# Optimization experiments

Hardware: AMD Instinct MI355X
Metric: run time of the kernel (lower is better)

Reference implementation:

```python
import jax, jax.numpy as jnp
import numpy as np

H = 512          # hidden_dim
AA = 21          # aa_num
NF = 6165        # num_features
B, N = 4, 2048   # graphs per batch, nodes per graph
LAMB = 1.0
OUT = 2


def gcn(x, adj, W, b):
    # Kipf GCN with self-loops on a (weighted) dense adjacency [B,n,n].
    n = adj.shape[-1]
    A = adj + jnp.eye(n, dtype=adj.dtype)
    d = jnp.sum(A, axis=-1)
    dinv = jax.lax.rsqrt(jnp.maximum(d, 1e-12))
    xw = x @ W                              # [B,n,Hout]
    msg = dinv[..., :, None] * (A @ (dinv[..., :, None] * xw))
    return msg + b


def hgpsl_pool(x, adj, att):
    # Node information score ||(I - D^-1 A) X||_1 (HGP-SL), top-k ratio 0.5,
    # then structure learning: row-softmax of pairwise attention + lamb*A.
    B_, n, h = x.shape
    d = jnp.sum(adj, axis=-1)
    dinv = 1.0 / jnp.maximum(d, 1.0)
    prop = (dinv[..., :, None] * adj) @ x
    score = jnp.sum(jnp.abs(x - prop), axis=-1)          # [B,n]
    k = n // 2
    _, idx = jax.lax.top_k(score, k)                     # [B,k]
    xk = jnp.take_along_axis(x, idx[:, :, None], axis=1)             # [B,k,h]
    a1 = jnp.take_along_axis(adj, idx[:, :, None], axis=1)           # [B,k,n]
    adjk = jnp.take_along_axis(a1, idx[:, None, :], axis=2)          # [B,k,k]
    # structure learning: e_ij = a^T [x_i || x_j] + lamb * A_ij
    li = xk @ att[:h]                                    # [B,k]
    lj = xk @ att[h:]                                    # [B,k]
    logits = li[:, :, None] + lj[:, None, :] + LAMB * adjk
    new_adj = jax.nn.softmax(logits, axis=-1)            # [B,k,k]
    return xk, new_adj


def readout(x):
    return jnp.concatenate([jnp.max(x, axis=1), jnp.mean(x, axis=1)], axis=-1)


def setup_inputs() -> dict:
    key = jax.random.key(0)
    ks = jax.random.split(key, 16)
    x = jax.random.normal(ks[0], (B, N, NF), dtype=jnp.float32)
    u = jax.random.uniform(ks[1], (B, N, N), dtype=jnp.float32)
    adj = (u < 0.008).astype(jnp.float32)
    adj = jnp.maximum(adj, jnp.swapaxes(adj, 1, 2))
    adj = adj * (1.0 - jnp.eye(N, dtype=jnp.float32))
    def w(k, shape):
        fan = shape[0]
        return jax.random.normal(k, shape, dtype=jnp.float32) / np.sqrt(fan)
    return {
        "x": x, "adj": adj,
        "lin1_W": w(ks[2], (NF - AA, H)), "lin1_b": jnp.zeros((H,), jnp.float32),
        "lin2_W": w(ks[3], (AA, AA)),     "lin2_b": jnp.zeros((AA,), jnp.float32),
        "conv1_W": w(ks[4], (H + AA, H)), "conv1_b": jnp.zeros((H,), jnp.float32),
        "conv2_W": w(ks[5], (H, H)),      "conv2_b": jnp.zeros((H,), jnp.float32),
        "conv3_W": w(ks[6], (H, H)),      "conv3_b": jnp.zeros((H,), jnp.float32),
        "att1": w(ks[7], (2 * H,)), "att2": w(ks[8], (2 * H,)),
        "fc1_W": w(ks[9], (2 * H, H)),    "fc1_b": jnp.zeros((H,), jnp.float32),
        "fc2_W": w(ks[10], (H, H // 2)),  "fc2_b": jnp.zeros((H // 2,), jnp.float32),
        "fc3_W": w(ks[11], (H // 2, OUT)),"fc3_b": jnp.zeros((OUT,), jnp.float32),
    }


def reference(x, adj, lin1_W, lin1_b, lin2_W, lin2_b, conv1_W, conv1_b,
              conv2_W, conv2_b, conv3_W, conv3_b, att1, att2,
              fc1_W, fc1_b, fc2_W, fc2_b, fc3_W, fc3_b):
    relu = jax.nn.relu
    x1 = relu(x[..., AA:] @ lin1_W + lin1_b)   # [B,N,H]
    x2 = relu(x[..., :AA] @ lin2_W + lin2_b)   # [B,N,AA]
    h = jnp.concatenate([x2, x1], axis=-1)     # [B,N,H+AA]
    h = relu(gcn(h, adj, conv1_W, conv1_b))
    h, adj1 = hgpsl_pool(h, adj, att1)         # N -> N/2
    r1 = readout(h)
    h = relu(gcn(h, adj1, conv2_W, conv2_b))
    h, adj2 = hgpsl_pool(h, adj1, att2)        # N/2 -> N/4
    r2 = readout(h)
    h = relu(gcn(h, adj2, conv3_W, conv3_b))
    r3 = readout(h)
    z = relu(r1) + relu(r2) + relu(r3)         # [B,2H]
    z = relu(z @ fc1_W + fc1_b)                # dropout is eval-mode identity
    z = relu(z @ fc2_W + fc2_b)
    return jax.nn.log_softmax(z @ fc3_W + fc3_b, axis=-1)
```

## Files before the change

kernel.cpp:

```cpp
#include <hip/hip_runtime.h>
#include <cstdint>
#include <cstddef>

typedef __bf16 bf16x8 __attribute__((ext_vector_type(8)));
typedef float f32x4 __attribute__((ext_vector_type(4)));

#define BUFSZ 24576

template <int MF>
__global__ __launch_bounds__(256) void gemm_mfma(
    const float* __restrict__ A, long lda, long sAb,
    const __bf16* __restrict__ Bp, long sBpb,
    float* __restrict__ C, long ldc, long sCb,
    int M, int N, int K,
    const float* __restrict__ bias,
    const float* __restrict__ rowscale,
    const float* __restrict__ addm, long sAddb, long ldadd,
    int do_relu)
{
  constexpr int BM = 32 * MF;
  __shared__ __align__(16) char smem[2 * BUFSZ];

  const int bz = blockIdx.z;
  const float* Ab = A + (size_t)bz * sAb;
  const __bf16* Bb = Bp + (size_t)bz * sBpb;
  float* Cb = C + (size_t)bz * sCb;

  int flat = blockIdx.y * gridDim.x + blockIdx.x;
  const int nwg = gridDim.x * gridDim.y;
  if ((nwg & 7) == 0) { const int q = nwg >> 3; flat = (flat & 7) * q + (flat >> 3); }
  const int col0 = (flat % gridDim.x) * 128;
  const int row0 = (flat / gridDim.x) * BM;

  const int t = threadIdx.x;
  const int w = t >> 6, l = t & 63;
  const int l16 = l & 15, lq = l >> 4;
  const int wr = w >> 1, wc = w & 1;
  const int T = K >> 5;

  const int s_row = t >> 2, s_oct = t & 3;
  const int a_off = (s_row >> 4) * 1024 + (s_oct * 16 + (s_row & 15)) * 16;
  const float* aptr = Ab + (size_t)(row0 + s_row) * lda + s_oct * 8;

  const __bf16* bsrc[4];
#pragma unroll
  for (int j = 0; j < 4; ++j) {
    const int c = t + 256 * j;
    const int g = c >> 7;
    bsrc[j] = Bb + ((size_t)((col0 >> 4) + g) * T) * 1024 + (size_t)(c & 127) * 8;
  }

  f32x4 acc[MF][4];
#pragma unroll
  for (int i = 0; i < MF; ++i)
#pragma unroll
    for (int j = 0; j < 4; ++j) acc[i][j] = (f32x4){0.f, 0.f, 0.f, 0.f};

  float a0r[8], a1r[8];
  bf16x8 bs0[4], bs1[4];

#define GA(dst, K0)                                                         \
  { const float* ap = aptr + (K0);                                          \
    _Pragma("unroll") for (int i = 0; i < 8; ++i) dst[i] = ap[i]; }

#define GB(dst, KT)                                                         \
  { _Pragma("unroll") for (int j = 0; j < 4; ++j)                           \
      dst[j] = *(const bf16x8*)(bsrc[j] + (size_t)(KT) * 1024); }

#define WA(buf, src)                                                        \
  { char* wb = smem + (buf) * BUFSZ; bf16x8 vh, vl;                         \
    _Pragma("unroll") for (int i = 0; i < 8; ++i) {                         \
      const __bf16 hh = (__bf16)src[i];                                     \
      vh[i] = hh; vl[i] = (__bf16)(src[i] - (float)hh); }                   \
    *(bf16x8*)(wb + a_off) = vh;                                            \
    *(bf16x8*)(wb + 4096 + a_off) = vl; }

#define WB(buf, src)                                                        \
  { char* wb = smem + (buf) * BUFSZ + 8192;                                 \
    _Pragma("unroll") for (int j = 0; j < 4; ++j)                           \
      *(bf16x8*)(wb + (t + 256 * j) * 16) = src[j]; }

#define COMPUTE(buf)                                                        \
  { const char* rb = smem + (buf) * BUFSZ;                                  \
    bf16x8 fbh[4], fbl[4];                                                  \
    _Pragma("unroll") for (int nf = 0; nf < 4; ++nf) {                      \
      const int g = wc * 4 + nf;                                            \
      fbh[nf] = *(const bf16x8*)(rb + 8192 + g * 2048 + l * 16);            \
      fbl[nf] = *(const bf16x8*)(rb + 8192 + g * 2048 + 1024 + l * 16); }   \
    _Pragma("unroll") for (int mf = 0; mf < MF; ++mf) {                     \
      const int fg = wr * MF + mf;                                          \
      bf16x8 fh = *(const bf16x8*)(rb + fg * 1024 + l * 16);                \
      bf16x8 fl = *(const bf16x8*)(rb + 4096 + fg * 1024 + l * 16);         \
      _Pragma("unroll") for (int nf = 0; nf < 4; ++nf) {                    \
        acc[mf][nf] = __builtin_amdgcn_mfma_f32_16x16x32_bf16(fl, fbh[nf], acc[mf][nf], 0, 0, 0); \
        acc[mf][nf] = __builtin_amdgcn_mfma_f32_16x16x32_bf16(fh, fbl[nf], acc[mf][nf], 0, 0, 0); \
        acc[mf][nf] = __builtin_amdgcn_mfma_f32_16x16x32_bf16(fh, fbh[nf], acc[mf][nf], 0, 0, 0); } } }

  GA(a0r, 0); GB(bs0, 0);
  WA(0, a0r); WB(0, bs0);
  if (T > 1) GA(a1r, 32);
  __syncthreads();

  int kt = 0;
  for (; kt + 2 <= T; kt += 2) {
    if (kt + 2 < T) GA(a0r, (kt + 2) * 32);
    GB(bs1, kt + 1);
    COMPUTE(0);
    WA(1, a1r); WB(1, bs1);
    __syncthreads();
    if (kt + 3 < T) GA(a1r, (kt + 3) * 32);
    if (kt + 2 < T) GB(bs0, kt + 2);
    COMPUTE(1);
    if (kt + 2 < T) { WA(0, a0r); WB(0, bs0); }
    __syncthreads();
  }
  if (kt < T) {
    COMPUTE(0);
  }
#undef GA
#undef GB
#undef WA
#undef WB
#undef COMPUTE

#pragma unroll
  for (int mf = 0; mf < MF; ++mf) {
#pragma unroll
    for (int r = 0; r < 4; ++r) {
      const int row = row0 + wr * (MF * 16) + mf * 16 + lq * 4 + r;
      const float rs = rowscale ? rowscale[(size_t)bz * M + row] : 1.f;
#pragma unroll
      for (int nf = 0; nf < 4; ++nf) {
        const int col = col0 + wc * 64 + nf * 16 + l16;
        float v = acc[mf][nf][r];
        if (addm) v += addm[(size_t)bz * sAddb + (size_t)row * ldadd + col];
        v *= rs;
        if (bias) v += bias[col];
        if (do_relu) v = fmaxf(v, 0.f);
        Cb[(size_t)row * ldc + col] = v;
      }
    }
  }
}

__global__ __launch_bounds__(64) void pack_b_kernel(
    const float* __restrict__ in, long sInb, int Kin, int Nin,
    __bf16* __restrict__ outP, long sPb, int T)
{
  const int kt = blockIdx.x, nf = blockIdx.y, b = blockIdx.z;
  const int l = threadIdx.x;
  const float* src = in + (size_t)b * sInb;
  const int col = nf * 16 + (l & 15);
  const int k0 = kt * 32 + (l >> 4) * 8;
  bf16x8 vh, vl;
#pragma unroll
  for (int j = 0; j < 8; ++j) {
    const int k = k0 + j;
    const float v = (k < Kin) ? src[(size_t)k * Nin + col] : 0.f;
    const __bf16 h = (__bf16)v;
    vh[j] = h; vl[j] = (__bf16)(v - (float)h);
  }
  __bf16* dst = outP + (size_t)b * sPb + ((size_t)nf * T + kt) * 1024 + l * 8;
  *(bf16x8*)dst = vh;
  *(bf16x8*)(dst + 512) = vl;
}

__global__ void lin2_kernel(const float* __restrict__ x, const float* __restrict__ W,
                            const float* __restrict__ b, float* __restrict__ h)
{
  int id = blockIdx.x * blockDim.x + threadIdx.x;
  if (id >= 4 * 2048 * 21) return;
  int row = id / 21, j = id % 21;
  const float* xr = x + (size_t)row * 6165;
  float acc = b[j];
  for (int i = 0; i < 21; ++i) acc = fmaf(xr[i], W[i * 21 + j], acc);
  h[(size_t)row * 544 + j] = fmaxf(acc, 0.f);
}

__global__ void pad_h_kernel(float* __restrict__ h)
{
  int id = blockIdx.x * blockDim.x + threadIdx.x;
  if (id >= 4 * 2048 * 11) return;
  int row = id / 11, c = 533 + id % 11;
  h[(size_t)row * 544 + c] = 0.f;
}

__global__ __launch_bounds__(256) void degrees_kernel(const float* __restrict__ adj,
                                                      float* __restrict__ dg,
                                                      float* __restrict__ dp)
{
  __shared__ float red[256];
  const int row = blockIdx.x;
  const int t = threadIdx.x;
  const float* ar = adj + (size_t)row * 2048;
  float s = 0.f;
  for (int j = t; j < 2048; j += 256) s += ar[j];
  red[t] = s; __syncthreads();
  for (int off = 128; off > 0; off >>= 1) {
    if (t < off) red[t] += red[t + off];
    __syncthreads();
  }
  if (t == 0) {
    float S = red[0];
    dg[row] = rsqrtf(fmaxf(S + 1.f, 1e-12f));
    dp[row] = 1.f / fmaxf(S, 1.f);
  }
}

__global__ __launch_bounds__(256) void conv1_msg_kernel(
    const float* __restrict__ adj, const float* __restrict__ xw,
    const float* __restrict__ dinv, const float* __restrict__ bias,
    float* __restrict__ out)
{
  __shared__ int nbr[2048];
  __shared__ float nval[2048];
  __shared__ int cnts[256];
  const int b = blockIdx.y, i = blockIdx.x, t = threadIdx.x;
  const float* ar = adj + ((size_t)(b * 2048 + i)) * 2048;
  int myj[8]; float myv[8]; int mc = 0;
  const int j0 = t * 8;
#pragma unroll
  for (int q = 0; q < 8; ++q) {
    float v = ar[j0 + q];
    if (v != 0.f) { myj[mc] = j0 + q; myv[mc] = v; ++mc; }
  }
  cnts[t] = mc; __syncthreads();
  for (int off = 1; off < 256; off <<= 1) {
    int v = cnts[t]; int add = (t >= off) ? cnts[t - off] : 0;
    __syncthreads();
    cnts[t] = v + add; __syncthreads();
  }
  const int base = cnts[t] - mc;
  const int total = cnts[255];
  for (int q = 0; q < mc; ++q) { nbr[base + q] = myj[q]; nval[base + q] = myv[q]; }
  __syncthreads();

  const float* xwb = xw + (size_t)b * 2048 * 512;
  const float* dv = dinv + b * 2048;
  float acc0 = 0.f, acc1 = 0.f;
  for (int n = 0; n < total; ++n) {
    const int j = nbr[n];
    const float w = nval[n] * dv[j];
    const float* xr = xwb + (size_t)j * 512;
    acc0 = fmaf(w, xr[t], acc0);
    acc1 = fmaf(w, xr[t + 256], acc1);
  }
  const float di = dv[i];
  const float* xi = xwb + (size_t)i * 512;
  acc0 = fmaf(di, xi[t], acc0);
  acc1 = fmaf(di, xi[t + 256], acc1);
  float* orow = out + ((size_t)(b * 2048 + i)) * 512;
  orow[t]       = fmaxf(di * acc0 + bias[t], 0.f);
  orow[t + 256] = fmaxf(di * acc1 + bias[t + 256], 0.f);
}

__global__ __launch_bounds__(256) void pool1_score_kernel(
    const float* __restrict__ adj, const float* __restrict__ h1,
    const float* __restrict__ dpool, float* __restrict__ score)
{
  __shared__ int nbr[2048];
  __shared__ float nval[2048];
  __shared__ int cnts[256];
  __shared__ float red[256];
  const int b = blockIdx.y, i = blockIdx.x, t = threadIdx.x;
  const float* ar = adj + ((size_t)(b * 2048 + i)) * 2048;
  int myj[8]; float myv[8]; int mc = 0;
  const int j0 = t * 8;
#pragma unroll
  for (int q = 0; q < 8; ++q) {
    float v = ar[j0 + q];
    if (v != 0.f) { myj[mc] = j0 + q; myv[mc] = v; ++mc; }
  }
  cnts[t] = mc; __syncthreads();
  for (int off = 1; off < 256; off <<= 1) {
    int v = cnts[t]; int add = (t >= off) ? cnts[t - off] : 0;
    __syncthreads();
    cnts[t] = v + add; __syncthreads();
  }
  const int base = cnts[t] - mc;
  const int total = cnts[255];
  for (int q = 0; q < mc; ++q) { nbr[base + q] = myj[q]; nval[base + q] = myv[q]; }
  __syncthreads();

  const float* hb = h1 + (size_t)b * 2048 * 512;
  float acc0 = 0.f, acc1 = 0.f;
  for (int n = 0; n < total; ++n) {
    const int j = nbr[n];
    const float w = nval[n];
    const float* xr = hb + (size_t)j * 512;
    acc0 = fmaf(w, xr[t], acc0);
    acc1 = fmaf(w, xr[t + 256], acc1);
  }
  const float dpi = dpool[b * 2048 + i];
  const float* hi = hb + (size_t)i * 512;
  float part = fabsf(hi[t] - dpi * acc0) + fabsf(hi[t + 256] - dpi * acc1);
  red[t] = part; __syncthreads();
  for (int off = 128; off > 0; off >>= 1) {
    if (t < off) red[t] += red[t + off];
    __syncthreads();
  }
  if (t == 0) score[b * 2048 + i] = red[0];
}

__global__ __launch_bounds__(1024) void topk_kernel(
    const float* __restrict__ score, int* __restrict__ idx_out, int n, int k)
{
  __shared__ unsigned long long key[2048];
  const unsigned b = blockIdx.x, t = threadIdx.x;
  const unsigned bd = blockDim.x;
  for (unsigned i = t; i < (unsigned)n; i += bd) {
    unsigned u = __float_as_uint(score[(size_t)b * n + i]);
    key[i] = ((unsigned long long)u << 32) | (unsigned)(~i);
  }
  __syncthreads();
  for (unsigned size = 2; size <= (unsigned)n; size <<= 1) {
    for (unsigned stride = size >> 1; stride > 0; stride >>= 1) {
      const unsigned i = (t / stride) * (stride * 2) + (t % stride);
      const unsigned ixj = i + stride;
      const bool up = ((i & size) == 0);
      unsigned long long a = key[i], c = key[ixj];
      if (up ? (a < c) : (a > c)) { key[i] = c; key[ixj] = a; }
      __syncthreads();
    }
  }
  const unsigned my = ~(unsigned)(key[t] & 0xFFFFFFFFull);
  __syncthreads();
  unsigned* arr = (unsigned*)key;
  arr[t] = my;
  __syncthreads();
  for (unsigned size = 2; size <= (unsigned)k; size <<= 1) {
    for (unsigned stride = size >> 1; stride > 0; stride >>= 1) {
      if (t < (unsigned)k / 2) {
        const unsigned i = (t / stride) * (stride * 2) + (t % stride);
        const unsigned ixj = i + stride;
        const bool up = ((i & size) == 0);
        unsigned a = arr[i], c = arr[ixj];
        if (up ? (a > c) : (a < c)) { arr[i] = c; arr[ixj] = a; }
      }
      __syncthreads();
    }
  }
  idx_out[(size_t)b * k + t] = (int)arr[t];
}

__global__ __launch_bounds__(256) void gather_li_kernel(
    const float* __restrict__ X, int src_n,
    const int* __restrict__ idx, int k,
    const float* __restrict__ att,
    float* __restrict__ xk, float* __restrict__ li, float* __restrict__ lj)
{
  __shared__ float redA[256], redB[256];
  const int b = blockIdx.y, r = blockIdx.x, t = threadIdx.x;
  const int g = idx[(size_t)b * k + r];
  const float* src = X + ((size_t)(b * src_n + g)) * 512;
  float* dst = xk + ((size_t)(b * k + r)) * 512;
  const float v0 = src[t], v1 = src[t + 256];
  dst[t] = v0; dst[t + 256] = v1;
  redA[t] = v0 * att[t] + v1 * att[t + 256];
  redB[t] = v0 * att[512 + t] + v1 * att[512 + t + 256];
  __syncthreads();
  for (int off = 128; off > 0; off >>= 1) {
    if (t < off) { redA[t] += redA[t + off]; redB[t] += redB[t + off]; }
    __syncthreads();
  }
  if (t == 0) { li[(size_t)b * k + r] = redA[0]; lj[(size_t)b * k + r] = redB[0]; }
}

__global__ __launch_bounds__(256) void slearn_kernel(
    const float* __restrict__ Asrc, int src_n,
    const int* __restrict__ idx, int k,
    const float* __restrict__ li, const float* __restrict__ lj,
    float* __restrict__ adj_out, float* __restrict__ dg, float* __restrict__ dp)
{
  __shared__ int gidx[1024];
  __shared__ float ljv[1024];
  __shared__ float lg[1024];
  __shared__ float red[256];
  const int b = blockIdx.y, r = blockIdx.x, t = threadIdx.x;
  for (int j = t; j < k; j += 256) { gidx[j] = idx[(size_t)b * k + j]; ljv[j] = lj[(size_t)b * k + j]; }
  __syncthreads();
  const int gi = gidx[r];
  const float lir = li[(size_t)b * k + r];
  const float* ar = Asrc + ((size_t)(b * src_n + gi)) * src_n;
  float mx = -3.4e38f;
  for (int j = t; j < k; j += 256) {
    float v = lir + ljv[j] + ar[gidx[j]];
    lg[j] = v; mx = fmaxf(mx, v);
  }
  red[t] = mx; __syncthreads();
  for (int off = 128; off > 0; off >>= 1) {
    if (t < off) red[t] = fmaxf(red[t], red[t + off]);
    __syncthreads();
  }
  const float m = red[0]; __syncthreads();
  float sm = 0.f;
  for (int j = t; j < k; j += 256) { float e = expf(lg[j] - m); lg[j] = e; sm += e; }
  red[t] = sm; __syncthreads();
  for (int off = 128; off > 0; off >>= 1) {
    if (t < off) red[t] += red[t + off];
    __syncthreads();
  }
  const float s = red[0]; __syncthreads();
  const float inv = 1.f / s;
  float ps = 0.f;
  float* orow = adj_out + ((size_t)(b * k + r)) * k;
  for (int j = t; j < k; j += 256) { float p = lg[j] * inv; orow[j] = p; ps += p; }
  red[t] = ps; __syncthreads();
  for (int off = 128; off > 0; off >>= 1) {
    if (t < off) red[t] += red[t + off];
    __syncthreads();
  }
  if (t == 0) {
    float S = red[0];
    dg[(size_t)b * k + r] = rsqrtf(fmaxf(S + 1.f, 1e-12f));
    dp[(size_t)b * k + r] = 1.f / fmaxf(S, 1.f);
  }
}

__global__ __launch_bounds__(512) void absdiff_kernel(
    const float* __restrict__ X, const float* __restrict__ P, float* __restrict__ score)
{
  __shared__ float red[512];
  const int row = blockIdx.x, t = threadIdx.x;
  float d = fabsf(X[(size_t)row * 512 + t] - P[(size_t)row * 512 + t]);
  red[t] = d; __syncthreads();
  for (int off = 256; off > 0; off >>= 1) {
    if (t < off) red[t] += red[t + off];
    __syncthreads();
  }
  if (t == 0) score[row] = red[0];
}

__global__ __launch_bounds__(512) void readout_part_kernel(
    const float* __restrict__ X, int nrows, int chunk_rows,
    float* __restrict__ partM, float* __restrict__ partS)
{
  const int b = blockIdx.x, chunk = blockIdx.y, c = threadIdx.x;
  const float* xb = X + ((size_t)b * nrows + (size_t)chunk * chunk_rows) * 512;
  float mx = -3.4e38f, sm = 0.f;
  for (int r = 0; r < chunk_rows; ++r) {
    float v = xb[(size_t)r * 512 + c];
    mx = fmaxf(mx, v); sm += v;
  }
  const size_t o = ((size_t)(b * gridDim.y + chunk)) * 512 + c;
  partM[o] = mx; partS[o] = sm;
}

__global__ __launch_bounds__(512) void readout_comb_kernel(
    const float* __restrict__ partM, const float* __restrict__ partS,
    int nchunks, int nrows, float* __restrict__ out)
{
  const int b = blockIdx.x, c = threadIdx.x;
  float mx = -3.4e38f, sm = 0.f;
  for (int q = 0; q < nchunks; ++q) {
    const size_t o = ((size_t)(b * nchunks + q)) * 512 + c;
    mx = fmaxf(mx, partM[o]); sm += partS[o];
  }
  out[(size_t)b * 1024 + c] = mx;
  out[(size_t)b * 1024 + 512 + c] = sm / (float)nrows;
}

__global__ __launch_bounds__(512) void final_mlp_kernel(
    const float* __restrict__ r1, const float* __restrict__ r2, const float* __restrict__ r3,
    const float* __restrict__ fc1W, const float* __restrict__ fc1b,
    const float* __restrict__ fc2W, const float* __restrict__ fc2b,
    const float* __restrict__ fc3W, const float* __restrict__ fc3b,
    float* __restrict__ out)
{
  __shared__ float z[1024];
  __shared__ float z1[512];
  __shared__ float z2[256];
  __shared__ float l[2];
  const int b = blockIdx.x, t = threadIdx.x;
  for (int c = t; c < 1024; c += 512)
    z[c] = fmaxf(r1[(size_t)b * 1024 + c], 0.f) + fmaxf(r2[(size_t)b * 1024 + c], 0.f)
         + fmaxf(r3[(size_t)b * 1024 + c], 0.f);
  __syncthreads();
  {
    float acc = fc1b[t];
    for (int i = 0; i < 1024; ++i) acc = fmaf(z[i], fc1W[(size_t)i * 512 + t], acc);
    z1[t] = fmaxf(acc, 0.f);
  }
  __syncthreads();
  if (t < 256) {
    float acc = fc2b[t];
    for (int i = 0; i < 512; ++i) acc = fmaf(z1[i], fc2W[(size_t)i * 256 + t], acc);
    z2[t] = fmaxf(acc, 0.f);
  }
  __syncthreads();
  if (t < 2) {
    float acc = fc3b[t];
    for (int i = 0; i < 256; ++i) acc = fmaf(z2[i], fc3W[(size_t)i * 2 + t], acc);
    l[t] = acc;
  }
  __syncthreads();
  if (t == 0) {
    float m = fmaxf(l[0], l[1]);
    float ls = m + logf(expf(l[0] - m) + expf(l[1] - m));
    out[b * 2 + 0] = l[0] - ls;
    out[b * 2 + 1] = l[1] - ls;
  }
}

extern "C" void kernel_launch(void* const* d_in, const int* in_sizes, int n_in,
                              void* d_out, int out_size, void* d_ws, size_t ws_size,
                              hipStream_t stream)
{
  (void)in_sizes; (void)n_in; (void)out_size; (void)ws_size;
  const float* x       = (const float*)d_in[0];
  const float* adj     = (const float*)d_in[1];
  const float* lin1_W  = (const float*)d_in[2];
  const float* lin1_b  = (const float*)d_in[3];
  const float* lin2_W  = (const float*)d_in[4];
  const float* lin2_b  = (const float*)d_in[5];
  const float* conv1_W = (const float*)d_in[6];
  const float* conv1_b = (const float*)d_in[7];
  const float* conv2_W = (const float*)d_in[8];
  const float* conv2_b = (const float*)d_in[9];
  const float* conv3_W = (const float*)d_in[10];
  const float* conv3_b = (const float*)d_in[11];
  const float* att1    = (const float*)d_in[12];
  const float* att2    = (const float*)d_in[13];
  const float* fc1_W   = (const float*)d_in[14];
  const float* fc1_b   = (const float*)d_in[15];
  const float* fc2_W   = (const float*)d_in[16];
  const float* fc2_b   = (const float*)d_in[17];
  const float* fc3_W   = (const float*)d_in[18];
  const float* fc3_b   = (const float*)d_in[19];
  float* ws  = (float*)d_ws;
  float* out = (float*)d_out;

  float* h     = ws + 0;
  float* adj1  = ws + 0;
  float* xw    = ws + 4456448;
  float* prop2 = xw;
  float* xk2   = ws + 4456448 + 2097152;
  float* adj2  = ws + 4456448 + 3145728;
  float* h1    = ws + 8650752;
  float* xk1   = ws + 12845056;
  float* xw3   = xk1;
  float* h3    = ws + 12845056 + 1048576;
  float* xw2   = ws + 14942208;
  float* h2    = ws + 17039360;
  float* S     = ws + 19136512;
  float* dinv_g1 = S;
  float* dinv_p1 = S + 8192;
  float* score1  = S + 16384;
  int*   idx1    = (int*)(S + 24576);
  float* li1     = S + 28672;
  float* lj1     = S + 32768;
  float* r1      = S + 36864;
  float* dinv_g2 = S + 40960;
  float* dinv_p2 = S + 45056;
  float* score2  = S + 49152;
  int*   idx2    = (int*)(S + 53248);
  float* li2     = S + 55296;
  float* lj2     = S + 57344;
  float* r2      = S + 59392;
  float* dinv_g3 = S + 63488;
  float* dinv_p3 = S + 65536;
  float* r3      = S + 67584;

  float* partM = ws + 4718592;
  float* partS = ws + 4718592 + 32768;

  __bf16* l1P  = (__bf16*)(ws + 8650752);
  __bf16* c1P  = (__bf16*)(ws + 12845056);
  __bf16* c2P  = (__bf16*)(ws + 17039360);
  __bf16* c3P  = (__bf16*)(ws + 4456448);
  __bf16* xw2P = (__bf16*)(ws + 12845056);
  __bf16* h2P  = (__bf16*)(ws + 8650752);
  __bf16* xw3P = (__bf16*)(ws + 10747904);

  pack_b_kernel<<<dim3(192, 32, 1), 64, 0, stream>>>(lin1_W, 0, 6144, 512, l1P, 0, 192);
  pack_b_kernel<<<dim3(17, 32, 1), 64, 0, stream>>>(conv1_W, 0, 533, 512, c1P, 0, 17);
  pack_b_kernel<<<dim3(16, 32, 1), 64, 0, stream>>>(conv2_W, 0, 512, 512, c2P, 0, 16);
  lin2_kernel<<<(4 * 2048 * 21 + 255) / 256, 256, 0, stream>>>(x, lin2_W, lin2_b, h);
  pad_h_kernel<<<(4 * 2048 * 11 + 255) / 256, 256, 0, stream>>>(h);
  gemm_mfma<2><<<dim3(4, 128, 1), 256, 0, stream>>>(x + 21, 6165, 0, l1P, 0,
      h + 21, 544, 0, 8192, 512, 6144, lin1_b, nullptr, nullptr, 0, 0, 1);
  degrees_kernel<<<8192, 256, 0, stream>>>(adj, dinv_g1, dinv_p1);
  gemm_mfma<2><<<dim3(4, 128, 1), 256, 0, stream>>>(h, 544, 0, c1P, 0,
      xw, 512, 0, 8192, 512, 544, nullptr, nullptr, nullptr, 0, 0, 0);
  conv1_msg_kernel<<<dim3(2048, 4), 256, 0, stream>>>(adj, xw, dinv_g1, conv1_b, h1);
  pool1_score_kernel<<<dim3(2048, 4), 256, 0, stream>>>(adj, h1, dinv_p1, score1);
  topk_kernel<<<4, 1024, 0, stream>>>(score1, idx1, 2048, 1024);
  gather_li_kernel<<<dim3(1024, 4), 256, 0, stream>>>(h1, 2048, idx1, 1024, att1, xk1, li1, lj1);
  slearn_kernel<<<dim3(1024, 4), 256, 0, stream>>>(adj, 2048, idx1, 1024, li1, lj1, adj1, dinv_g2, dinv_p2);
  readout_part_kernel<<<dim3(4, 16), 512, 0, stream>>>(xk1, 1024, 64, partM, partS);
  readout_comb_kernel<<<4, 512, 0, stream>>>(partM, partS, 16, 1024, r1);
  gemm_mfma<2><<<dim3(4, 64, 1), 256, 0, stream>>>(xk1, 512, 0, c2P, 0,
      xw2, 512, 0, 4096, 512, 512, nullptr, dinv_g2, nullptr, 0, 0, 0);
  pack_b_kernel<<<dim3(32, 32, 4), 64, 0, stream>>>(xw2, 524288, 1024, 512, xw2P, 1048576, 32);
  gemm_mfma<2><<<dim3(4, 16, 4), 256, 0, stream>>>(adj1, 1024, 1048576, xw2P, 1048576,
      h2, 512, 524288, 1024, 512, 1024, conv2_b, dinv_g2, xw2, 524288, 512, 1);
  pack_b_kernel<<<dim3(32, 32, 4), 64, 0, stream>>>(h2, 524288, 1024, 512, h2P, 1048576, 32);
  gemm_mfma<2><<<dim3(4, 16, 4), 256, 0, stream>>>(adj1, 1024, 1048576, h2P, 1048576,
      prop2, 512, 524288, 1024, 512, 1024, nullptr, dinv_p2, nullptr, 0, 0, 0);
  absdiff_kernel<<<4096, 512, 0, stream>>>(h2, prop2, score2);
  pack_b_kernel<<<dim3(16, 32, 1), 64, 0, stream>>>(conv3_W, 0, 512, 512, c3P, 0, 16);
  topk_kernel<<<4, 512, 0, stream>>>(score2, idx2, 1024, 512);
  gather_li_kernel<<<dim3(512, 4), 256, 0, stream>>>(h2, 1024, idx2, 512, att2, xk2, li2, lj2);
  slearn_kernel<<<dim3(512, 4), 256, 0, stream>>>(adj1, 1024, idx2, 512, li2, lj2, adj2, dinv_g3, dinv_p3);
  readout_part_kernel<<<dim3(4, 16), 512, 0, stream>>>(xk2, 512, 32, partM, partS);
  readout_comb_kernel<<<4, 512, 0, stream>>>(partM, partS, 16, 512, r2);
  gemm_mfma<2><<<dim3(4, 32, 1), 256, 0, stream>>>(xk2, 512, 0, c3P, 0,
      xw3, 512, 0, 2048, 512, 512, nullptr, dinv_g3, nullptr, 0, 0, 0);
  pack_b_kernel<<<dim3(16, 32, 4), 64, 0, stream>>>(xw3, 262144, 512, 512, xw3P, 524288, 16);
  gemm_mfma<2><<<dim3(4, 8, 4), 256, 0, stream>>>(adj2, 512, 262144, xw3P, 524288,
      h3, 512, 262144, 512, 512, 512, conv3_b, dinv_g3, xw3, 262144, 512, 1);
  readout_part_kernel<<<dim3(4, 16), 512, 0, stream>>>(h3, 512, 32, partM, partS);
  readout_comb_kernel<<<4, 512, 0, stream>>>(partM, partS, 16, 512, r3);
  final_mlp_kernel<<<4, 512, 0, stream>>>(r1, r2, r3, fc1_W, fc1_b, fc2_W, fc2_b,
                                          fc3_W, fc3_b, out);
}
```

Before: 731.6 us.

## Replace sparse conv1/pool1 gather kernels with dense MFMA GEMMs over the adjacency

Drops the per-row sparse neighbor-compaction kernels for the first GCN message pass and the pool-1 score. Both are now done as dense batched MFMA GEMMs of adj times a packed xw or h1, with dinv applied as a row scale and an absdiff kernel computing the score. A new template parameter NT=2 skips the low-half A split product, since adj holds exact 0/1 values. The B-operand prefetch is also moved one stage earlier. This trades irregular gathers for dense tensor-core work, roughly 8.6 GFLOP per pass plus pack kernels, when the adjacency is only about 1.6% dense.

```diff
diff --git a/kernel.cpp b/kernel.cpp
--- a/kernel.cpp
+++ b/kernel.cpp
@@ -7,7 +7,7 @@
 
 #define BUFSZ 24576
 
-template <int MF>
+template <int MF, int NT>
 __global__ __launch_bounds__(256) void gemm_mfma(
     const float* __restrict__ A, long lda, long sAb,
     const __bf16* __restrict__ Bp, long sBpb,
@@ -59,8 +59,8 @@
   float a0r[8], a1r[8];
   bf16x8 bs0[4], bs1[4];
 
-#define GA(dst, K0)                                                         \
-  { const float* ap = aptr + (K0);                                          \
+#define GA(dst, KT)                                                         \
+  { const float* ap = aptr + (size_t)(KT) * 32;                             \
     _Pragma("unroll") for (int i = 0; i < 8; ++i) dst[i] = ap[i]; }
 
 #define GB(dst, KT)                                                         \
@@ -71,9 +71,10 @@
   { char* wb = smem + (buf) * BUFSZ; bf16x8 vh, vl;                         \
     _Pragma("unroll") for (int i = 0; i < 8; ++i) {                         \
       const __bf16 hh = (__bf16)src[i];                                     \
-      vh[i] = hh; vl[i] = (__bf16)(src[i] - (float)hh); }                   \
+      vh[i] = hh;                                                           \
+      if (NT == 3) vl[i] = (__bf16)(src[i] - (float)hh); }                  \
     *(bf16x8*)(wb + a_off) = vh;                                            \
-    *(bf16x8*)(wb + 4096 + a_off) = vl; }
+    if (NT == 3) *(bf16x8*)(wb + 4096 + a_off) = vl; }
 
 #define WB(buf, src)                                                        \
   { char* wb = smem + (buf) * BUFSZ + 8192;                                 \
@@ -90,26 +91,26 @@
     _Pragma("unroll") for (int mf = 0; mf < MF; ++mf) {                     \
       const int fg = wr * MF + mf;                                          \
       bf16x8 fh = *(const bf16x8*)(rb + fg * 1024 + l * 16);                \
-      bf16x8 fl = *(const bf16x8*)(rb + 4096 + fg * 1024 + l * 16);         \
+      bf16x8 fl;                                                            \
+      if (NT == 3) fl = *(const bf16x8*)(rb + 4096 + fg * 1024 + l * 16);   \
       _Pragma("unroll") for (int nf = 0; nf < 4; ++nf) {                    \
-        acc[mf][nf] = __builtin_amdgcn_mfma_f32_16x16x32_bf16(fl, fbh[nf], acc[mf][nf], 0, 0, 0); \
+        if (NT == 3)                                                        \
+          acc[mf][nf] = __builtin_amdgcn_mfma_f32_16x16x32_bf16(fl, fbh[nf], acc[mf][nf], 0, 0, 0); \
         acc[mf][nf] = __builtin_amdgcn_mfma_f32_16x16x32_bf16(fh, fbl[nf], acc[mf][nf], 0, 0, 0); \
         acc[mf][nf] = __builtin_amdgcn_mfma_f32_16x16x32_bf16(fh, fbh[nf], acc[mf][nf], 0, 0, 0); } } }
 
   GA(a0r, 0); GB(bs0, 0);
   WA(0, a0r); WB(0, bs0);
-  if (T > 1) GA(a1r, 32);
+  if (T > 1) { GA(a1r, 1); GB(bs1, 1); }
   __syncthreads();
 
   int kt = 0;
   for (; kt + 2 <= T; kt += 2) {
-    if (kt + 2 < T) GA(a0r, (kt + 2) * 32);
-    GB(bs1, kt + 1);
+    if (kt + 2 < T) { GA(a0r, kt + 2); GB(bs0, kt + 2); }
     COMPUTE(0);
     WA(1, a1r); WB(1, bs1);
     __syncthreads();
-    if (kt + 3 < T) GA(a1r, (kt + 3) * 32);
-    if (kt + 2 < T) GB(bs0, kt + 2);
+    if (kt + 3 < T) { GA(a1r, kt + 3); GB(bs1, kt + 3); }
     COMPUTE(1);
     if (kt + 2 < T) { WA(0, a0r); WB(0, bs0); }
     __syncthreads();
@@ -205,101 +206,6 @@
     dg[row] = rsqrtf(fmaxf(S + 1.f, 1e-12f));
     dp[row] = 1.f / fmaxf(S, 1.f);
   }
-}
-
-__global__ __launch_bounds__(256) void conv1_msg_kernel(
-    const float* __restrict__ adj, const float* __restrict__ xw,
-    const float* __restrict__ dinv, const float* __restrict__ bias,
-    float* __restrict__ out)
-{
-  __shared__ int nbr[2048];
-  __shared__ float nval[2048];
-  __shared__ int cnts[256];
-  const int b = blockIdx.y, i = blockIdx.x, t = threadIdx.x;
-  const float* ar = adj + ((size_t)(b * 2048 + i)) * 2048;
-  int myj[8]; float myv[8]; int mc = 0;
-  const int j0 = t * 8;
-#pragma unroll
-  for (int q = 0; q < 8; ++q) {
-    float v = ar[j0 + q];
-    if (v != 0.f) { myj[mc] = j0 + q; myv[mc] = v; ++mc; }
-  }
-  cnts[t] = mc; __syncthreads();
-  for (int off = 1; off < 256; off <<= 1) {
-    int v = cnts[t]; int add = (t >= off) ? cnts[t - off] : 0;
-    __syncthreads();
-    cnts[t] = v + add; __syncthreads();
-  }
-  const int base = cnts[t] - mc;
-  const int total = cnts[255];
-  for (int q = 0; q < mc; ++q) { nbr[base + q] = myj[q]; nval[base + q] = myv[q]; }
-  __syncthreads();
-
-  const float* xwb = xw + (size_t)b * 2048 * 512;
-  const float* dv = dinv + b * 2048;
-  float acc0 = 0.f, acc1 = 0.f;
-  for (int n = 0; n < total; ++n) {
-    const int j = nbr[n];
-    const float w = nval[n] * dv[j];
-    const float* xr = xwb + (size_t)j * 512;
-    acc0 = fmaf(w, xr[t], acc0);
-    acc1 = fmaf(w, xr[t + 256], acc1);
-  }
-  const float di = dv[i];
-  const float* xi = xwb + (size_t)i * 512;
-  acc0 = fmaf(di, xi[t], acc0);
-  acc1 = fmaf(di, xi[t + 256], acc1);
-  float* orow = out + ((size_t)(b * 2048 + i)) * 512;
-  orow[t]       = fmaxf(di * acc0 + bias[t], 0.f);
-  orow[t + 256] = fmaxf(di * acc1 + bias[t + 256], 0.f);
-}
-
-__global__ __launch_bounds__(256) void pool1_score_kernel(
-    const float* __restrict__ adj, const float* __restrict__ h1,
-    const float* __restrict__ dpool, float* __restrict__ score)
-{
-  __shared__ int nbr[2048];
-  __shared__ float nval[2048];
-  __shared__ int cnts[256];
-  __shared__ float red[256];
-  const int b = blockIdx.y, i = blockIdx.x, t = threadIdx.x;
-  const float* ar = adj + ((size_t)(b * 2048 + i)) * 2048;
-  int myj[8]; float myv[8]; int mc = 0;
-  const int j0 = t * 8;
-#pragma unroll
-  for (int q = 0; q < 8; ++q) {
-    float v = ar[j0 + q];
-    if (v != 0.f) { myj[mc] = j0 + q; myv[mc] = v; ++mc; }
-  }
-  cnts[t] = mc; __syncthreads();
-  for (int off = 1; off < 256; off <<= 1) {
-    int v = cnts[t]; int add = (t >= off) ? cnts[t - off] : 0;
-    __syncthreads();
-    cnts[t] = v + add; __syncthreads();
-  }
-  const int base = cnts[t] - mc;
-  const int total = cnts[255];
-  for (int q = 0; q < mc; ++q) { nbr[base + q] = myj[q]; nval[base + q] = myv[q]; }
-  __syncthreads();
-
-  const float* hb = h1 + (size_t)b * 2048 * 512;
-  float acc0 = 0.f, acc1 = 0.f;
-  for (int n = 0; n < total; ++n) {
-    const int j = nbr[n];
-    const float w = nval[n];
-    const float* xr = hb + (size_t)j * 512;
-    acc0 = fmaf(w, xr[t], acc0);
-    acc1 = fmaf(w, xr[t + 256], acc1);
-  }
-  const float dpi = dpool[b * 2048 + i];
-  const float* hi = hb + (size_t)i * 512;
-  float part = fabsf(hi[t] - dpi * acc0) + fabsf(hi[t + 256] - dpi * acc1);
-  red[t] = part; __syncthreads();
-  for (int off = 128; off > 0; off >>= 1) {
-    if (t < off) red[t] += red[t + off];
-    __syncthreads();
-  }
-  if (t == 0) score[b * 2048 + i] = red[0];
 }
 
 __global__ __launch_bounds__(1024) void topk_kernel(
@@ -532,8 +438,8 @@
 
   float* h     = ws + 0;
   float* adj1  = ws + 0;
-  float* xw    = ws + 4456448;
-  float* prop2 = xw;
+  float* xwd   = ws + 4456448;
+  float* prop2 = ws + 4456448;
   float* xk2   = ws + 4456448 + 2097152;
   float* adj2  = ws + 4456448 + 3145728;
   float* h1    = ws + 8650752;
@@ -566,6 +472,9 @@
 
   __bf16* l1P  = (__bf16*)(ws + 8650752);
   __bf16* c1P  = (__bf16*)(ws + 12845056);
+  __bf16* xwdP = (__bf16*)(ws + 12845056);
+  __bf16* h1P  = (__bf16*)(ws + 4456448);
+  float*  prop1 = ws + 12845056;
   __bf16* c2P  = (__bf16*)(ws + 17039360);
   __bf16* c3P  = (__bf16*)(ws + 4456448);
   __bf16* xw2P = (__bf16*)(ws + 12845056);
@@ -577,25 +486,30 @@
   pack_b_kernel<<<dim3(16, 32, 1), 64, 0, stream>>>(conv2_W, 0, 512, 512, c2P, 0, 16);
   lin2_kernel<<<(4 * 2048 * 21 + 255) / 256, 256, 0, stream>>>(x, lin2_W, lin2_b, h);
   pad_h_kernel<<<(4 * 2048 * 11 + 255) / 256, 256, 0, stream>>>(h);
-  gemm_mfma<2><<<dim3(4, 128, 1), 256, 0, stream>>>(x + 21, 6165, 0, l1P, 0,
+  gemm_mfma<2, 3><<<dim3(4, 128, 1), 256, 0, stream>>>(x + 21, 6165, 0, l1P, 0,
       h + 21, 544, 0, 8192, 512, 6144, lin1_b, nullptr, nullptr, 0, 0, 1);
   degrees_kernel<<<8192, 256, 0, stream>>>(adj, dinv_g1, dinv_p1);
-  gemm_mfma<2><<<dim3(4, 128, 1), 256, 0, stream>>>(h, 544, 0, c1P, 0,
-      xw, 512, 0, 8192, 512, 544, nullptr, nullptr, nullptr, 0, 0, 0);
-  conv1_msg_kernel<<<dim3(2048, 4), 256, 0, stream>>>(adj, xw, dinv_g1, conv1_b, h1);
-  pool1_score_kernel<<<dim3(2048, 4), 256, 0, stream>>>(adj, h1, dinv_p1, score1);
+  gemm_mfma<2, 3><<<dim3(4, 128, 1), 256, 0, stream>>>(h, 544, 0, c1P, 0,
+      xwd, 512, 0, 8192, 512, 544, nullptr, dinv_g1, nullptr, 0, 0, 0);
+  pack_b_kernel<<<dim3(64, 32, 4), 64, 0, stream>>>(xwd, 1048576, 2048, 512, xwdP, 2097152, 64);
+  gemm_mfma<2, 2><<<dim3(4, 32, 4), 256, 0, stream>>>(adj, 2048, 4194304, xwdP, 2097152,
+      h1, 512, 1048576, 2048, 512, 2048, conv1_b, dinv_g1, xwd, 1048576, 512, 1);
+  pack_b_kernel<<<dim3(64, 32, 4), 64, 0, stream>>>(h1, 1048576, 2048, 512, h1P, 2097152, 64);
+  gemm_mfma<2, 2><<<dim3(4, 32, 4), 256, 0, stream>>>(adj, 2048, 4194304, h1P, 2097152,
+      prop1, 512, 1048576, 2048, 512, 2048, nullptr, dinv_p1, nullptr, 0, 0, 0);
+  absdiff_kernel<<<8192, 512, 0, stream>>>(h1, prop1, score1);
   topk_kernel<<<4, 1024, 0, stream>>>(score1, idx1, 2048, 1024);
   gather_li_kernel<<<dim3(1024, 4), 256, 0, stream>>>(h1, 2048, idx1, 1024, att1, xk1, li1, lj1);
   slearn_kernel<<<dim3(1024, 4), 256, 0, stream>>>(adj, 2048, idx1, 1024, li1, lj1, adj1, dinv_g2, dinv_p2);
   readout_part_kernel<<<dim3(4, 16), 512, 0, stream>>>(xk1, 1024, 64, partM, partS);
   readout_comb_kernel<<<4, 512, 0, stream>>>(partM, partS, 16, 1024, r1);
-  gemm_mfma<2><<<dim3(4, 64, 1), 256, 0, stream>>>(xk1, 512, 0, c2P, 0,
+  gemm_mfma<2, 3><<<dim3(4, 64, 1), 256, 0, stream>>>(xk1, 512, 0, c2P, 0,
       xw2, 512, 0, 4096, 512, 512, nullptr, dinv_g2, nullptr, 0, 0, 0);
   pack_b_kernel<<<dim3(32, 32, 4), 64, 0, stream>>>(xw2, 524288, 1024, 512, xw2P, 1048576, 32);
-  gemm_mfma<2><<<dim3(4, 16, 4), 256, 0, stream>>>(adj1, 1024, 1048576, xw2P, 1048576,
+  gemm_mfma<2, 3><<<dim3(4, 16, 4), 256, 0, stream>>>(adj1, 1024, 1048576, xw2P, 1048576,
       h2, 512, 524288, 1024, 512, 1024, conv2_b, dinv_g2, xw2, 524288, 512, 1);
   pack_b_kernel<<<dim3(32, 32, 4), 64, 0, stream>>>(h2, 524288, 1024, 512, h2P, 1048576, 32);
-  gemm_mfma<2><<<dim3(4, 16, 4), 256, 0, stream>>>(adj1, 1024, 1048576, h2P, 1048576,
+  gemm_mfma<2, 3><<<dim3(4, 16, 4), 256, 0, stream>>>(adj1, 1024, 1048576, h2P, 1048576,
       prop2, 512, 524288, 1024, 512, 1024, nullptr, dinv_p2, nullptr, 0, 0, 0);
   absdiff_kernel<<<4096, 512, 0, stream>>>(h2, prop2, score2);
   pack_b_kernel<<<dim3(16, 32, 1), 64, 0, stream>>>(conv3_W, 0, 512, 512, c3P, 0, 16);
@@ -604,10 +518,10 @@
   slearn_kernel<<<dim3(512, 4), 256, 0, stream>>>(adj1, 1024, idx2, 512, li2, lj2, adj2, dinv_g3, dinv_p3);
   readout_part_kernel<<<dim3(4, 16), 512, 0, stream>>>(xk2, 512, 32, partM, partS);
   readout_comb_kernel<<<4, 512, 0, stream>>>(partM, partS, 16, 512, r2);
-  gemm_mfma<2><<<dim3(4, 32, 1), 256, 0, stream>>>(xk2, 512, 0, c3P, 0,
+  gemm_mfma<2, 3><<<dim3(4, 32, 1), 256, 0, stream>>>(xk2, 512, 0, c3P, 0,
       xw3, 512, 0, 2048, 512, 512, nullptr, dinv_g3, nullptr, 0, 0, 0);
   pack_b_kernel<<<dim3(16, 32, 4), 64, 0, stream>>>(xw3, 262144, 512, 512, xw3P, 524288, 16);
-  gemm_mfma<2><<<dim3(4, 8, 4), 256, 0, stream>>>(adj2, 512, 262144, xw3P, 524288,
+  gemm_mfma<2, 3><<<dim3(4, 8, 4), 256, 0, stream>>>(adj2, 512, 262144, xw3P, 524288,
       h3, 512, 262144, 512, 512, 512, conv3_b, dinv_g3, xw3, 262144, 512, 1);
   readout_part_kernel<<<dim3(4, 16), 512, 0, stream>>>(h3, 512, 32, partM, partS);
   readout_comb_kernel<<<4, 512, 0, stream>>>(partM, partS, 16, 512, r3);
```

New measurement: 780.5 us. 6.7% more time.
